# Performance work log

Measured on AMD Instinct MI355X. Metric: run time of the kernel, lower is better.

## Reference

```python
import jax, jax.numpy as jnp
import numpy as np

N = 100000      # nodes
E = 1600000     # edges
D_IN = 128      # input_dim
H = 256         # hidden_dim
L = 3           # num_layers
B = 64          # graphs per batch
BN_EPS = 1e-5


def setup_inputs() -> dict:
    key = jax.random.key(0)
    ks = jax.random.split(key, 8)
    x = jax.random.normal(ks[0], (N, D_IN), dtype=jnp.float32)
    edge_index = jax.random.randint(ks[1], (2, E), 0, N, dtype=jnp.int32)
    batch = jnp.sort(jax.random.randint(ks[2], (N,), 0, B, dtype=jnp.int32))
    W0 = jax.random.normal(ks[3], (D_IN, H), dtype=jnp.float32) / np.sqrt(D_IN)
    W_rest = jax.random.normal(ks[4], (L - 1, H, H), dtype=jnp.float32) / np.sqrt(H)
    b = jax.random.normal(ks[5], (L, H), dtype=jnp.float32) * 0.01
    gamma = 1.0 + jax.random.normal(ks[6], (L, H), dtype=jnp.float32) * 0.01
    beta = jax.random.normal(ks[7], (L, H), dtype=jnp.float32) * 0.01
    return {"x": x, "W0": W0, "W_rest": W_rest, "b": b, "gamma": gamma,
            "beta": beta, "edge_index": edge_index, "batch": batch}


def reference(x, W0, W_rest, b, gamma, beta, edge_index, batch):
    src, dst = edge_index[0], edge_index[1]
    # GCN symmetric normalization with self-loops: deg = in-degree + 1
    deg = jax.ops.segment_sum(jnp.ones((E,), x.dtype), dst, num_segments=N) + 1.0
    dis = jax.lax.rsqrt(deg)                   # deg^{-1/2}, [N]
    enorm = dis[src] * dis[dst]                # per-edge norm, [E]
    self_norm = (dis * dis)[:, None]           # self-loop norm = 1/deg, [N,1]

    def gcn_bn_relu(h, W, bb, g, be):
        h = h @ W                                                  # [N,H]
        agg = jax.ops.segment_sum(h[src] * enorm[:, None], dst, num_segments=N)
        h = agg + h * self_norm + bb                               # self-loop + bias
        # BatchNorm1d (training mode: batch stats, biased variance)
        m = h.mean(axis=0)
        v = h.var(axis=0)
        h = (h - m) * jax.lax.rsqrt(v + BN_EPS) * g + be
        return jax.nn.relu(h)                                      # dropout = identity (eval)

    h = gcn_bn_relu(x, W0, b[0], gamma[0], beta[0])
    for i in range(L - 1):
        h = gcn_bn_relu(h, W_rest[i], b[i + 1], gamma[i + 1], beta[i + 1])

    # segment pooling per graph (att_pool in the original is dead code: not returned)
    counts = jax.ops.segment_sum(jnp.ones((N,), h.dtype), batch, num_segments=B)
    mean_pool = jax.ops.segment_sum(h, batch, num_segments=B) / counts[:, None]
    max_pool = jax.ops.segment_max(h, batch, num_segments=B)
    return jnp.concatenate([mean_pool, max_pool], axis=1)          # [B, 2H]
```

## Files before the change

### kernel.cpp

```cpp
#include <hip/hip_runtime.h>
#include <hip/hip_bf16.h>
#include <stdint.h>


#define NN 100000
#define EE 1600000
#define BB 64
#define MPAD 100096
#define NBM (MPAD / 256)

typedef __attribute__((ext_vector_type(8))) short short8;
typedef __attribute__((ext_vector_type(4))) float f32x4;

__device__ __forceinline__ float bflo(uint32_t v){ return __uint_as_float(v << 16); }
__device__ __forceinline__ float bfhi(uint32_t v){ return __uint_as_float(v & 0xffff0000u); }
__device__ __forceinline__ uint32_t bfrne(float x){
  uint32_t u = __float_as_uint(x);
  return (u + 0x7fffu + ((u >> 16) & 1u)) >> 16;
}
__device__ __forceinline__ uint32_t bfpack(float a, float b){ return bfrne(a) | (bfrne(b) << 16); }
__device__ __forceinline__ float phi(long long p){
  return __uint_as_float((uint32_t)((unsigned long long)p >> 32));
}

__device__ __forceinline__ void gload_lds16(const void* g, void* l){
  __builtin_amdgcn_global_load_lds(
      (const __attribute__((address_space(1))) uint32_t*)g,
      (__attribute__((address_space(3))) uint32_t*)l, 16, 0, 0);
}

__global__ void k_deg(const int* __restrict__ dst, int* __restrict__ degi){
  for (int e = blockIdx.x * blockDim.x + threadIdx.x; e < EE; e += gridDim.x * blockDim.x)
    atomicAdd(&degi[dst[e]], 1);
}

__global__ void k_scan1(const int* __restrict__ degi, int* __restrict__ rp, int* __restrict__ bsum,
                        float* __restrict__ dis){
  __shared__ int lds[256];
  int b = blockIdx.x, t = threadIdx.x;
  int base = b * 1024 + t * 4;
  int v0 = (base + 0 < NN) ? degi[base + 0] : 0;
  int v1 = (base + 1 < NN) ? degi[base + 1] : 0;
  int v2 = (base + 2 < NN) ? degi[base + 2] : 0;
  int v3 = (base + 3 < NN) ? degi[base + 3] : 0;
  if (base + 0 < NN) dis[base + 0] = rsqrtf((float)v0 + 1.0f);
  if (base + 1 < NN) dis[base + 1] = rsqrtf((float)v1 + 1.0f);
  if (base + 2 < NN) dis[base + 2] = rsqrtf((float)v2 + 1.0f);
  if (base + 3 < NN) dis[base + 3] = rsqrtf((float)v3 + 1.0f);
  int s = v0 + v1 + v2 + v3;
  lds[t] = s; __syncthreads();
  for (int off = 1; off < 256; off <<= 1){
    int x = (t >= off) ? lds[t - off] : 0; __syncthreads();
    lds[t] += x; __syncthreads();
  }
  int excl = lds[t] - s;
  if (t == 255) bsum[b] = lds[255];
  if (base + 0 < NN) rp[base + 0] = excl;
  if (base + 1 < NN) rp[base + 1] = excl + v0;
  if (base + 2 < NN) rp[base + 2] = excl + v0 + v1;
  if (base + 3 < NN) rp[base + 3] = excl + v0 + v1 + v2;
}

__global__ void k_scan2(int* __restrict__ bsum, int nb){
  if (blockIdx.x == 0 && threadIdx.x == 0){
    int run = 0;
    for (int i = 0; i < nb; ++i){ int t = bsum[i]; bsum[i] = run; run += t; }
  }
}

__global__ void k_scan3(int* __restrict__ rp, int* __restrict__ cursor, const int* __restrict__ bsum){
  int b = blockIdx.x, t = threadIdx.x;
  int add = bsum[b];
  int base = b * 1024 + t * 4;
  #pragma unroll
  for (int j = 0; j < 4; ++j){
    int i = base + j;
    if (i < NN){ int v = rp[i] + add; rp[i] = v; cursor[i] = v; }
  }
  if (b == 0 && t == 0) rp[NN] = EE;
}

__global__ void k_fill(const int* __restrict__ src, const int* __restrict__ dst,
                       const float* __restrict__ dis, int* __restrict__ cursor,
                       long long* __restrict__ cp){
  for (int e = blockIdx.x * blockDim.x + threadIdx.x; e < EE; e += gridDim.x * blockDim.x){
    int s = src[e], d = dst[e];
    int pos = atomicAdd(&cursor[d], 1);
    float nrm = dis[s] * dis[d];
    long long v = (long long)(unsigned int)s | ((long long)(unsigned int)__float_as_uint(nrm) << 32);
    cp[pos] = v;
  }
}

__global__ void k_sort(const int* __restrict__ rp, long long* __restrict__ cp){
  int wid = (blockIdx.x * blockDim.x + threadIdx.x) >> 6;
  int lane = threadIdx.x & 63;
  if (wid >= NN) return;
  int beg = rp[wid], end = rp[wid + 1];
  int d = end - beg;
  if (d <= 1) return;
  if (d <= 64){
    long long key = (lane < d) ? cp[beg + lane] : 0x7fffffffffffffffLL;
    #pragma unroll
    for (int k = 2; k <= 64; k <<= 1){
      #pragma unroll
      for (int j = k >> 1; j > 0; j >>= 1){
        long long other = __shfl_xor(key, j);
        bool up = ((lane & k) == 0);
        bool keepMin = (((lane & j) == 0) == up);
        bool take = keepMin ? (other < key) : (other > key);
        if (take) key = other;
      }
    }
    if (lane < d) cp[beg + lane] = key;
  } else if (lane == 0){
    for (int i = beg + 1; i < end; ++i){
      long long k2 = cp[i];
      int j = i - 1;
      while (j >= beg && cp[j] > k2){ cp[j + 1] = cp[j]; --j; }
      cp[j + 1] = k2;
    }
  }
}

__global__ void k_prep(const float* __restrict__ W0, const float* __restrict__ Wr,
                       uint16_t* __restrict__ Wt0, uint16_t* __restrict__ Wt1,
                       uint16_t* __restrict__ Wt2,
                       const float* __restrict__ x, uint32_t* __restrict__ Xb){
  int b = blockIdx.x;
  if (b < 640){
    int i = b * 256 + threadIdx.x;
    if (i < 32768){
      int c = i >> 7, k = i & 127;
      Wt0[i] = (uint16_t)bfrne(W0[k * 256 + c]);
    } else if (i < 32768 + 131072){
      int j = i - 32768;
      int m = j >> 16, jj = j & 65535;
      int c = jj >> 8, k = jj & 255;
      uint16_t v = (uint16_t)bfrne(Wr[m * 65536 + k * 256 + c]);
      if (m == 0) Wt1[jj] = v; else Wt2[jj] = v;
    }
  } else {
    int i = (b - 640) * 256 + threadIdx.x;
    if (i >= MPAD * 64) return;
    int row = i >> 6;
    uint32_t r = 0u;
    if (row < NN){
      int col = (i & 63) * 2;
      r = bfpack(x[row * 128 + col], x[row * 128 + col + 1]);
    }
    Xb[i] = r;
  }
}

__global__ void k_agg256(const uint2* __restrict__ Xin, const int* __restrict__ rp,
                         const long long* __restrict__ cp, const float* __restrict__ dis,
                         uint2* __restrict__ Xout){
  int lane = threadIdx.x & 63;
  int slot = threadIdx.x >> 6;
  int row0 = blockIdx.x * 16 + slot;
  for (int rr = 0; rr < 4; ++rr){
    int row = row0 + rr * 4;
    if (row >= NN){
      if (row < MPAD)
        __builtin_nontemporal_store(0ull, (unsigned long long*)&Xout[(size_t)row * 64 + lane]);
      continue;
    }
    int beg = rp[row], end = rp[row + 1];
    float a0 = 0.f, a1 = 0.f, a2 = 0.f, a3 = 0.f;
    int e = beg;
    for (; e + 8 <= end; e += 8){
      long long p[8]; uint2 v[8];
      #pragma unroll
      for (int u = 0; u < 8; ++u) p[u] = __builtin_nontemporal_load(&cp[e + u]);
      #pragma unroll
      for (int u = 0; u < 8; ++u) v[u] = Xin[(size_t)(int)p[u] * 64 + lane];
      #pragma unroll
      for (int u = 0; u < 8; ++u){
        float w = phi(p[u]);
        a0 += w * bflo(v[u].x); a1 += w * bfhi(v[u].x);
        a2 += w * bflo(v[u].y); a3 += w * bfhi(v[u].y);
      }
    }
    for (; e < end; ++e){
      long long p0 = __builtin_nontemporal_load(&cp[e]);
      float w = phi(p0);
      uint2 v = Xin[(size_t)(int)p0 * 64 + lane];
      a0 += w * bflo(v.x); a1 += w * bfhi(v.x);
      a2 += w * bflo(v.y); a3 += w * bfhi(v.y);
    }
    float dv = dis[row]; float sn = dv * dv;
    uint2 vs = Xin[(size_t)row * 64 + lane];
    a0 += sn * bflo(vs.x); a1 += sn * bfhi(vs.x);
    a2 += sn * bflo(vs.y); a3 += sn * bfhi(vs.y);
    unsigned long long o = (unsigned long long)bfpack(a0, a1)
                         | ((unsigned long long)bfpack(a2, a3) << 32);
    __builtin_nontemporal_store(o, (unsigned long long*)&Xout[(size_t)row * 64 + lane]);
  }
}

__global__ void k_agg128(const uint2* __restrict__ Xin, const int* __restrict__ rp,
                         const long long* __restrict__ cp, const float* __restrict__ dis,
                         uint2* __restrict__ Xout){
  int lane = threadIdx.x & 63;
  int half = lane >> 5, j = lane & 31;
  int slot = threadIdx.x >> 6;
  int row0 = blockIdx.x * 16 + slot;
  for (int rr = 0; rr < 4; ++rr){
    int row = row0 + rr * 4;
    if (row >= NN){
      if (row < MPAD && half == 0)
        __builtin_nontemporal_store(0ull, (unsigned long long*)&Xout[(size_t)row * 32 + j]);
      continue;
    }
    int beg = rp[row], end = rp[row + 1];
    float a0 = 0.f, a1 = 0.f, a2 = 0.f, a3 = 0.f;
    int e = beg;
    for (; e + 8 <= end; e += 8){
      long long p[4]; uint2 v[4];
      #pragma unroll
      for (int u = 0; u < 4; ++u) p[u] = __builtin_nontemporal_load(&cp[e + u * 2 + half]);
      #pragma unroll
      for (int u = 0; u < 4; ++u) v[u] = Xin[(size_t)(int)p[u] * 32 + j];
      #pragma unroll
      for (int u = 0; u < 4; ++u){
        float w = phi(p[u]);
        a0 += w * bflo(v[u].x); a1 += w * bfhi(v[u].x);
        a2 += w * bflo(v[u].y); a3 += w * bfhi(v[u].y);
      }
    }
    for (; e < end; e += 2){
      int idx = e + half;
      bool ok = idx < end;
      long long p0 = cp[ok ? idx : end - 1];
      float w = ok ? phi(p0) : 0.f;
      uint2 v = Xin[(size_t)(int)p0 * 32 + j];
      a0 += w * bflo(v.x); a1 += w * bfhi(v.x);
      a2 += w * bflo(v.y); a3 += w * bfhi(v.y);
    }
    a0 += __shfl_xor(a0, 32); a1 += __shfl_xor(a1, 32);
    a2 += __shfl_xor(a2, 32); a3 += __shfl_xor(a3, 32);
    if (half == 0){
      float dv = dis[row]; float sn = dv * dv;
      uint2 vs = Xin[(size_t)row * 32 + j];
      a0 += sn * bflo(vs.x); a1 += sn * bfhi(vs.x);
      a2 += sn * bflo(vs.y); a3 += sn * bfhi(vs.y);
      unsigned long long o = (unsigned long long)bfpack(a0, a1)
                           | ((unsigned long long)bfpack(a2, a3) << 32);
      __builtin_nontemporal_store(o, (unsigned long long*)&Xout[(size_t)row * 32 + j]);
    }
  }
}

template<int K>
__global__ __launch_bounds__(512) void k_gemm(const uint16_t* __restrict__ A,
                                              const uint16_t* __restrict__ Bt,
                                              uint32_t* __restrict__ Cb,
                                              float* __restrict__ pstat){
  __shared__ __align__(16) uint16_t lA[2][8192];
  __shared__ __align__(16) uint16_t lB[2][4096];
  __shared__ float lp[8][128];
  int tid = threadIdx.x;
  int l = tid & 63;
  int bm = blockIdx.x, bn = blockIdx.y;

  f32x4 acc[4][4];
  #pragma unroll
  for (int m = 0; m < 4; ++m)
    #pragma unroll
    for (int n = 0; n < 4; ++n){ f32x4 z = {0.f,0.f,0.f,0.f}; acc[m][n] = z; }

  int w = tid >> 6, wr = w >> 1, wc = w & 1;
  int rbase = wr * 64, cbase = wc * 64;
  int lrow = l & 15, lk8 = l >> 4;

  auto stage = [&](int kt, int buf){
    #pragma unroll
    for (int i = 0; i < 2; ++i){
      int c = i * 512 + tid;
      int k8 = c >> 8, r = c & 255;
      size_t ga = (size_t)(bm * 256 + r) * K + kt * 32 + k8 * 8;
      gload_lds16((const char*)(A + ga), (char*)&lA[buf][c * 8]);
    }
    int k8b = tid >> 7, rb = tid & 127;
    size_t gb = (size_t)(bn * 128 + rb) * K + kt * 32 + k8b * 8;
    gload_lds16((const char*)(Bt + gb), (char*)&lB[buf][tid * 8]);
  };

  stage(0, 0);
  __syncthreads();
  constexpr int NT = K / 32;
  for (int kt = 0; kt < NT; ++kt){
    int cur = kt & 1;
    if (kt + 1 < NT) stage(kt + 1, cur ^ 1);
    short8 afr[4], bfr[4];
    #pragma unroll
    for (int m = 0; m < 4; ++m)
      afr[m] = *(const short8*)&lA[cur][(lk8 * 256 + rbase + m * 16 + lrow) * 8];
    #pragma unroll
    for (int n = 0; n < 4; ++n)
      bfr[n] = *(const short8*)&lB[cur][(lk8 * 128 + cbase + n * 16 + lrow) * 8];
    #pragma unroll
    for (int m = 0; m < 4; ++m)
      #pragma unroll
      for (int n = 0; n < 4; ++n)
        acc[m][n] = __builtin_amdgcn_mfma_f32_16x16x32_bf16(afr[m], bfr[n], acc[m][n], 0, 0, 0);
    __syncthreads();
  }

  int grow0 = bm * 256 + rbase + (l >> 4) * 4;
  int gcol0 = bn * 128 + cbase + (l & 15);
  uint16_t* C16 = (uint16_t*)Cb;
  float sa[4] = {0.f,0.f,0.f,0.f}, sb[4] = {0.f,0.f,0.f,0.f};
  #pragma unroll
  for (int m = 0; m < 4; ++m){
    #pragma unroll
    for (int n = 0; n < 4; ++n){
      int col = gcol0 + n * 16;
      int r0 = grow0 + m * 16;
      f32x4 v = acc[m][n];
      #pragma unroll
      for (int q = 0; q < 4; ++q){
        C16[(size_t)(r0 + q) * 256 + col] = (uint16_t)bfrne(v[q]);
        sa[n] += v[q]; sb[n] += v[q] * v[q];
      }
    }
  }
  #pragma unroll
  for (int n = 0; n < 4; ++n){
    sa[n] += __shfl_xor(sa[n], 16); sa[n] += __shfl_xor(sa[n], 32);
    sb[n] += __shfl_xor(sb[n], 16); sb[n] += __shfl_xor(sb[n], 32);
  }
  if (l < 16){
    #pragma unroll
    for (int n = 0; n < 4; ++n){
      lp[w][n * 16 + l] = sa[n];
      lp[w][64 + n * 16 + l] = sb[n];
    }
  }
  __syncthreads();
  if (tid < 256){
    int kind = tid >> 7, c = tid & 127;
    int wc2 = c >> 6, cc = c & 63;
    float v = lp[wc2][kind * 64 + cc] + lp[2 + wc2][kind * 64 + cc]
            + lp[4 + wc2][kind * 64 + cc] + lp[6 + wc2][kind * 64 + cc];
    pstat[(size_t)(bm * 2 + bn) * 256 + kind * 128 + c] = v;
  }
}

__global__ void k_finalize(const float* __restrict__ pstat, const float* __restrict__ gamma,
                           const float* __restrict__ beta, float* __restrict__ ss){
  int c = threadIdx.x;
  int bn = c >> 7, lc = c & 127;
  double s[8], s2[8];
  #pragma unroll
  for (int j = 0; j < 8; ++j){ s[j] = 0.; s2[j] = 0.; }
  int bm = 0;
  for (; bm + 8 <= NBM; bm += 8){
    #pragma unroll
    for (int j = 0; j < 8; ++j){
      const float* p = pstat + (size_t)((bm + j) * 2 + bn) * 256;
      s[j]  += (double)p[lc];
      s2[j] += (double)p[128 + lc];
    }
  }
  for (; bm < NBM; ++bm){
    const float* p = pstat + (size_t)(bm * 2 + bn) * 256;
    s[0]  += (double)p[lc];
    s2[0] += (double)p[128 + lc];
  }
  double S  = ((s[0]+s[1])+(s[2]+s[3]))  + ((s[4]+s[5])+(s[6]+s[7]));
  double S2 = ((s2[0]+s2[1])+(s2[2]+s2[3])) + ((s2[4]+s2[5])+(s2[6]+s2[7]));
  double mean = S / (double)NN;
  double var  = S2 / (double)NN - mean * mean;
  float rstd = rsqrtf((float)var + 1e-5f);
  float sc = gamma[c] * rstd;
  ss[c] = sc;
  ss[256 + c] = beta[c] - (float)mean * sc;
}

__global__ void k_bnapply(const uint4* __restrict__ Y, const float* __restrict__ ss,
                          uint4* __restrict__ X){
  int i = blockIdx.x * 256 + threadIdx.x;
  if (i >= MPAD * 32) return;
  uint4 v = Y[i];
  int c0 = (i & 31) * 8;
  float r0 = fmaxf(bflo(v.x) * ss[c0 + 0] + ss[256 + c0 + 0], 0.f);
  float r1 = fmaxf(bfhi(v.x) * ss[c0 + 1] + ss[256 + c0 + 1], 0.f);
  float r2 = fmaxf(bflo(v.y) * ss[c0 + 2] + ss[256 + c0 + 2], 0.f);
  float r3 = fmaxf(bfhi(v.y) * ss[c0 + 3] + ss[256 + c0 + 3], 0.f);
  float r4 = fmaxf(bflo(v.z) * ss[c0 + 4] + ss[256 + c0 + 4], 0.f);
  float r5 = fmaxf(bfhi(v.z) * ss[c0 + 5] + ss[256 + c0 + 5], 0.f);
  float r6 = fmaxf(bflo(v.w) * ss[c0 + 6] + ss[256 + c0 + 6], 0.f);
  float r7 = fmaxf(bfhi(v.w) * ss[c0 + 7] + ss[256 + c0 + 7], 0.f);
  uint4 o;
  o.x = bfpack(r0, r1); o.y = bfpack(r2, r3);
  o.z = bfpack(r4, r5); o.w = bfpack(r6, r7);
  X[i] = o;
}

__device__ __forceinline__ int segfind(const int* __restrict__ batch, int g){
  if (g <= 0) return 0;
  if (g >= BB) return NN;
  int lo = 0, hi = NN;
  while (lo < hi){ int mid = (lo + hi) >> 1; if (batch[mid] < g) lo = mid + 1; else hi = mid; }
  return lo;
}

__global__ void k_poolpart(const uint32_t* __restrict__ Y, const float* __restrict__ ss,
                           const int* __restrict__ batch, float* __restrict__ pb){
  int g = blockIdx.x, c = blockIdx.y, t = threadIdx.x;
  float sc0 = ss[2*t], sc1 = ss[2*t+1];
  float sh0 = ss[256+2*t], sh1 = ss[256+2*t+1];
  int s = segfind(batch, g), e = segfind(batch, g + 1);
  int len = e - s;
  int c0 = s + (int)(((long long)len * c) >> 3);
  int c1 = s + (int)(((long long)len * (c + 1)) >> 3);
  float sm0 = 0.f, sm1 = 0.f, mx0 = -1e30f, mx1 = -1e30f;
  #pragma unroll 4
  for (int r = c0; r < c1; ++r){
    uint32_t v = Y[(size_t)r * 128 + t];
    float a  = fmaxf(bflo(v) * sc0 + sh0, 0.f);
    float b2 = fmaxf(bfhi(v) * sc1 + sh1, 0.f);
    sm0 += a; sm1 += b2;
    mx0 = fmaxf(mx0, a); mx1 = fmaxf(mx1, b2);
  }
  float* p = pb + (size_t)(g * 8 + c) * 512;
  p[2 * t] = sm0; p[2 * t + 1] = sm1;
  p[256 + 2 * t] = mx0; p[256 + 2 * t + 1] = mx1;
}

__global__ void k_poolred(const float* __restrict__ pb, const int* __restrict__ batch,
                          float* __restrict__ out){
  int g = blockIdx.x, cc = threadIdx.x;
  float s = 0.f, m = -1e30f;
  #pragma unroll
  for (int c = 0; c < 8; ++c){
    const float* p = pb + (size_t)(g * 8 + c) * 512;
    s += p[cc];
    m = fmaxf(m, p[256 + cc]);
  }
  float inv = 1.0f / (float)(segfind(batch, g + 1) - segfind(batch, g));
  out[g * 512 + cc] = s * inv;
  out[g * 512 + 256 + cc] = m;
}

extern "C" void kernel_launch(void* const* d_in, const int* in_sizes, int n_in,
                              void* d_out, int out_size, void* d_ws, size_t ws_size,
                              hipStream_t stream){
  const float* x     = (const float*)d_in[0];
  const float* W0    = (const float*)d_in[1];
  const float* Wr    = (const float*)d_in[2];
  const float* gamma = (const float*)d_in[4];
  const float* beta  = (const float*)d_in[5];
  const int*   ei    = (const int*)d_in[6];
  const int*   batch = (const int*)d_in[7];
  const int* esrc = ei;
  const int* edst = ei + EE;
  float* out = (float*)d_out;

  char* base = (char*)d_ws;
  size_t off = 0;
  auto alloc = [&](size_t b)->char*{
    char* p = base + off; off = (off + b + 255) & ~(size_t)255; return p;
  };
  uint32_t* Xbuf = (uint32_t*)alloc((size_t)MPAD * 256 * 2);
  uint32_t* Xagg = (uint32_t*)alloc((size_t)MPAD * 256 * 2);
  uint32_t* Y    = (uint32_t*)alloc((size_t)MPAD * 256 * 2);
  uint16_t* Wt0  = (uint16_t*)alloc(256 * 128 * 2);
  uint16_t* Wt1  = (uint16_t*)alloc(256 * 256 * 2);
  uint16_t* Wt2  = (uint16_t*)alloc(256 * 256 * 2);
  int*   degi   = (int*)  alloc((size_t)NN * 4);
  float* dis    = (float*)alloc((size_t)NN * 4);
  int*   rp     = (int*)  alloc((size_t)(NN + 1) * 4);
  int*   cursor = (int*)  alloc((size_t)NN * 4);
  int*   bsum   = (int*)  alloc(128 * 4);
  long long* cp = (long long*)alloc((size_t)EE * 8);
  float* pstat  = (float*)alloc((size_t)NBM * 2 * 256 * 4);
  float* ss     = (float*)alloc(512 * 4);
  float* pb     = (float*)alloc((size_t)BB * 8 * 512 * 4);

  hipMemsetAsync(degi, 0, (size_t)NN * 4, stream);
  k_deg<<<2048, 256, 0, stream>>>(edst, degi);
  k_scan1<<<98, 256, 0, stream>>>(degi, rp, bsum, dis);
  k_scan2<<<1, 1, 0, stream>>>(bsum, 98);
  k_scan3<<<98, 256, 0, stream>>>(rp, cursor, bsum);
  k_fill<<<2048, 256, 0, stream>>>(esrc, edst, dis, cursor, cp);
  k_sort<<<NN / 4, 256, 0, stream>>>(rp, cp);
  k_prep<<<640 + MPAD * 64 / 256, 256, 0, stream>>>(W0, Wr, Wt0, Wt1, Wt2, x, Xbuf);

  k_agg128<<<MPAD / 16, 256, 0, stream>>>((const uint2*)Xbuf, rp, cp, dis, (uint2*)Xagg);
  k_gemm<128><<<dim3(NBM, 2), 512, 0, stream>>>((const uint16_t*)Xagg, Wt0, Y, pstat);
  k_finalize<<<1, 256, 0, stream>>>(pstat, gamma + 0, beta + 0, ss);
  k_bnapply<<<MPAD * 32 / 256, 256, 0, stream>>>((const uint4*)Y, ss, (uint4*)Xbuf);

  k_agg256<<<MPAD / 16, 256, 0, stream>>>((const uint2*)Xbuf, rp, cp, dis, (uint2*)Xagg);
  k_gemm<256><<<dim3(NBM, 2), 512, 0, stream>>>((const uint16_t*)Xagg, Wt1, Y, pstat);
  k_finalize<<<1, 256, 0, stream>>>(pstat, gamma + 256, beta + 256, ss);
  k_bnapply<<<MPAD * 32 / 256, 256, 0, stream>>>((const uint4*)Y, ss, (uint4*)Xbuf);

  k_agg256<<<MPAD / 16, 256, 0, stream>>>((const uint2*)Xbuf, rp, cp, dis, (uint2*)Xagg);
  k_gemm<256><<<dim3(NBM, 2), 512, 0, stream>>>((const uint16_t*)Xagg, Wt2, Y, pstat);
  k_finalize<<<1, 256, 0, stream>>>(pstat, gamma + 512, beta + 512, ss);

  k_poolpart<<<dim3(BB, 8), 128, 0, stream>>>(Y, ss, batch, pb);
  k_poolred<<<BB, 256, 0, stream>>>(pb, batch, out);
}
```

Baseline: 849.9 us.

## Fuse BatchNorm+ReLU into aggregation gather and drop separate bnapply and scan2 kernels

Removes the standalone k_bnapply pass by applying the per-channel scale/shift and ReLU (with bf16 rounding to match) on each gathered neighbor value inside k_agg256. It also folds the single-thread k_scan2 block-prefix into k_scan3 through a per-block LDS reduction, and switches cp loads from nontemporal to normal loads. This saves one full read/write pass of the 100k x 256 activation per layer and two launches. The cost is redundant BN math on every gathered edge (about 16x per node) plus an extra activation buffer.

```diff
diff --git a/kernel.cpp b/kernel.cpp
--- a/kernel.cpp
+++ b/kernel.cpp
@@ -21,6 +21,10 @@
 __device__ __forceinline__ uint32_t bfpack(float a, float b){ return bfrne(a) | (bfrne(b) << 16); }
 __device__ __forceinline__ float phi(long long p){
   return __uint_as_float((uint32_t)((unsigned long long)p >> 32));
+}
+__device__ __forceinline__ float bnr(float y, float sc, float sh){
+  float t = fmaxf(y * sc + sh, 0.f);
+  return __uint_as_float(bfrne(t) << 16);
 }
 
 __device__ __forceinline__ void gload_lds16(const void* g, void* l){
@@ -61,16 +65,16 @@
   if (base + 3 < NN) rp[base + 3] = excl + v0 + v1 + v2;
 }
 
-__global__ void k_scan2(int* __restrict__ bsum, int nb){
-  if (blockIdx.x == 0 && threadIdx.x == 0){
-    int run = 0;
-    for (int i = 0; i < nb; ++i){ int t = bsum[i]; bsum[i] = run; run += t; }
-  }
-}
-
 __global__ void k_scan3(int* __restrict__ rp, int* __restrict__ cursor, const int* __restrict__ bsum){
+  __shared__ int red[256];
   int b = blockIdx.x, t = threadIdx.x;
-  int add = bsum[b];
+  red[t] = (t < b && t < 98) ? bsum[t] : 0;
+  __syncthreads();
+  for (int off = 128; off > 0; off >>= 1){
+    if (t < off) red[t] += red[t + off];
+    __syncthreads();
+  }
+  int add = red[0];
   int base = b * 1024 + t * 4;
   #pragma unroll
   for (int j = 0; j < 4; ++j){
@@ -153,11 +157,13 @@
   }
 }
 
-__global__ void k_agg256(const uint2* __restrict__ Xin, const int* __restrict__ rp,
+__global__ void k_agg256(const uint2* __restrict__ Yin, const int* __restrict__ rp,
                          const long long* __restrict__ cp, const float* __restrict__ dis,
-                         uint2* __restrict__ Xout){
+                         const float* __restrict__ ss, uint2* __restrict__ Xout){
   int lane = threadIdx.x & 63;
   int slot = threadIdx.x >> 6;
+  float sc0 = ss[lane*4+0], sc1 = ss[lane*4+1], sc2 = ss[lane*4+2], sc3 = ss[lane*4+3];
+  float sh0 = ss[256+lane*4+0], sh1 = ss[256+lane*4+1], sh2 = ss[256+lane*4+2], sh3 = ss[256+lane*4+3];
   int row0 = blockIdx.x * 16 + slot;
   for (int rr = 0; rr < 4; ++rr){
     int row = row0 + rr * 4;
@@ -172,27 +178,33 @@
     for (; e + 8 <= end; e += 8){
       long long p[8]; uint2 v[8];
       #pragma unroll
-      for (int u = 0; u < 8; ++u) p[u] = __builtin_nontemporal_load(&cp[e + u]);
-      #pragma unroll
-      for (int u = 0; u < 8; ++u) v[u] = Xin[(size_t)(int)p[u] * 64 + lane];
+      for (int u = 0; u < 8; ++u) p[u] = cp[e + u];
+      #pragma unroll
+      for (int u = 0; u < 8; ++u) v[u] = Yin[(size_t)(int)p[u] * 64 + lane];
       #pragma unroll
       for (int u = 0; u < 8; ++u){
         float w = phi(p[u]);
-        a0 += w * bflo(v[u].x); a1 += w * bfhi(v[u].x);
-        a2 += w * bflo(v[u].y); a3 += w * bfhi(v[u].y);
+        a0 += w * bnr(bflo(v[u].x), sc0, sh0);
+        a1 += w * bnr(bfhi(v[u].x), sc1, sh1);
+        a2 += w * bnr(bflo(v[u].y), sc2, sh2);
+        a3 += w * bnr(bfhi(v[u].y), sc3, sh3);
       }
     }
     for (; e < end; ++e){
-      long long p0 = __builtin_nontemporal_load(&cp[e]);
+      long long p0 = cp[e];
       float w = phi(p0);
-      uint2 v = Xin[(size_t)(int)p0 * 64 + lane];
-      a0 += w * bflo(v.x); a1 += w * bfhi(v.x);
-      a2 += w * bflo(v.y); a3 += w * bfhi(v.y);
+      uint2 v = Yin[(size_t)(int)p0 * 64 + lane];
+      a0 += w * bnr(bflo(v.x), sc0, sh0);
+      a1 += w * bnr(bfhi(v.x), sc1, sh1);
+      a2 += w * bnr(bflo(v.y), sc2, sh2);
+      a3 += w * bnr(bfhi(v.y), sc3, sh3);
     }
     float dv = dis[row]; float sn = dv * dv;
-    uint2 vs = Xin[(size_t)row * 64 + lane];
-    a0 += sn * bflo(vs.x); a1 += sn * bfhi(vs.x);
-    a2 += sn * bflo(vs.y); a3 += sn * bfhi(vs.y);
+    uint2 vs = Yin[(size_t)row * 64 + lane];
+    a0 += sn * bnr(bflo(vs.x), sc0, sh0);
+    a1 += sn * bnr(bfhi(vs.x), sc1, sh1);
+    a2 += sn * bnr(bflo(vs.y), sc2, sh2);
+    a3 += sn * bnr(bfhi(vs.y), sc3, sh3);
     unsigned long long o = (unsigned long long)bfpack(a0, a1)
                          | ((unsigned long long)bfpack(a2, a3) << 32);
     __builtin_nontemporal_store(o, (unsigned long long*)&Xout[(size_t)row * 64 + lane]);
@@ -219,7 +231,7 @@
     for (; e + 8 <= end; e += 8){
       long long p[4]; uint2 v[4];
       #pragma unroll
-      for (int u = 0; u < 4; ++u) p[u] = __builtin_nontemporal_load(&cp[e + u * 2 + half]);
+      for (int u = 0; u < 4; ++u) p[u] = cp[e + u * 2 + half];
       #pragma unroll
       for (int u = 0; u < 4; ++u) v[u] = Xin[(size_t)(int)p[u] * 32 + j];
       #pragma unroll
@@ -377,26 +389,6 @@
   float sc = gamma[c] * rstd;
   ss[c] = sc;
   ss[256 + c] = beta[c] - (float)mean * sc;
-}
-
-__global__ void k_bnapply(const uint4* __restrict__ Y, const float* __restrict__ ss,
-                          uint4* __restrict__ X){
-  int i = blockIdx.x * 256 + threadIdx.x;
-  if (i >= MPAD * 32) return;
-  uint4 v = Y[i];
-  int c0 = (i & 31) * 8;
-  float r0 = fmaxf(bflo(v.x) * ss[c0 + 0] + ss[256 + c0 + 0], 0.f);
-  float r1 = fmaxf(bfhi(v.x) * ss[c0 + 1] + ss[256 + c0 + 1], 0.f);
-  float r2 = fmaxf(bflo(v.y) * ss[c0 + 2] + ss[256 + c0 + 2], 0.f);
-  float r3 = fmaxf(bfhi(v.y) * ss[c0 + 3] + ss[256 + c0 + 3], 0.f);
-  float r4 = fmaxf(bflo(v.z) * ss[c0 + 4] + ss[256 + c0 + 4], 0.f);
-  float r5 = fmaxf(bfhi(v.z) * ss[c0 + 5] + ss[256 + c0 + 5], 0.f);
-  float r6 = fmaxf(bflo(v.w) * ss[c0 + 6] + ss[256 + c0 + 6], 0.f);
-  float r7 = fmaxf(bfhi(v.w) * ss[c0 + 7] + ss[256 + c0 + 7], 0.f);
-  uint4 o;
-  o.x = bfpack(r0, r1); o.y = bfpack(r2, r3);
-  o.z = bfpack(r4, r5); o.w = bfpack(r6, r7);
-  X[i] = o;
 }
 
 __device__ __forceinline__ int segfind(const int* __restrict__ batch, int g){
@@ -464,9 +456,10 @@
   auto alloc = [&](size_t b)->char*{
     char* p = base + off; off = (off + b + 255) & ~(size_t)255; return p;
   };
-  uint32_t* Xbuf = (uint32_t*)alloc((size_t)MPAD * 256 * 2);
+  uint32_t* Xbuf = (uint32_t*)alloc((size_t)MPAD * 128 * 2);
   uint32_t* Xagg = (uint32_t*)alloc((size_t)MPAD * 256 * 2);
-  uint32_t* Y    = (uint32_t*)alloc((size_t)MPAD * 256 * 2);
+  uint32_t* Y1   = (uint32_t*)alloc((size_t)MPAD * 256 * 2);
+  uint32_t* Y2   = (uint32_t*)alloc((size_t)MPAD * 256 * 2);
   uint16_t* Wt0  = (uint16_t*)alloc(256 * 128 * 2);
   uint16_t* Wt1  = (uint16_t*)alloc(256 * 256 * 2);
   uint16_t* Wt2  = (uint16_t*)alloc(256 * 256 * 2);
@@ -483,26 +476,23 @@
   hipMemsetAsync(degi, 0, (size_t)NN * 4, stream);
   k_deg<<<2048, 256, 0, stream>>>(edst, degi);
   k_scan1<<<98, 256, 0, stream>>>(degi, rp, bsum, dis);
-  k_scan2<<<1, 1, 0, stream>>>(bsum, 98);
   k_scan3<<<98, 256, 0, stream>>>(rp, cursor, bsum);
   k_fill<<<2048, 256, 0, stream>>>(esrc, edst, dis, cursor, cp);
   k_sort<<<NN / 4, 256, 0, stream>>>(rp, cp);
   k_prep<<<640 + MPAD * 64 / 256, 256, 0, stream>>>(W0, Wr, Wt0, Wt1, Wt2, x, Xbuf);
 
   k_agg128<<<MPAD / 16, 256, 0, stream>>>((const uint2*)Xbuf, rp, cp, dis, (uint2*)Xagg);
-  k_gemm<128><<<dim3(NBM, 2), 512, 0, stream>>>((const uint16_t*)Xagg, Wt0, Y, pstat);
+  k_gemm<128><<<dim3(NBM, 2), 512, 0, stream>>>((const uint16_t*)Xagg, Wt0, Y1, pstat);
   k_finalize<<<1, 256, 0, stream>>>(pstat, gamma + 0, beta + 0, ss);
-  k_bnapply<<<MPAD * 32 / 256, 256, 0, stream>>>((const uint4*)Y, ss, (uint4*)Xbuf);
-
-  k_agg256<<<MPAD / 16, 256, 0, stream>>>((const uint2*)Xbuf, rp, cp, dis, (uint2*)Xagg);
-  k_gemm<256><<<dim3(NBM, 2), 512, 0, stream>>>((const uint16_t*)Xagg, Wt1, Y, pstat);
+
+  k_agg256<<<MPAD / 16, 256, 0, stream>>>((const uint2*)Y1, rp, cp, dis, ss, (uint2*)Xagg);
+  k_gemm<256><<<dim3(NBM, 2), 512, 0, stream>>>((const uint16_t*)Xagg, Wt1, Y2, pstat);
   k_finalize<<<1, 256, 0, stream>>>(pstat, gamma + 256, beta + 256, ss);
-  k_bnapply<<<MPAD * 32 / 256, 256, 0, stream>>>((const uint4*)Y, ss, (uint4*)Xbuf);
-
-  k_agg256<<<MPAD / 16, 256, 0, stream>>>((const uint2*)Xbuf, rp, cp, dis, (uint2*)Xagg);
-  k_gemm<256><<<dim3(NBM, 2), 512, 0, stream>>>((const uint16_t*)Xagg, Wt2, Y, pstat);
+
+  k_agg256<<<MPAD / 16, 256, 0, stream>>>((const uint2*)Y2, rp, cp, dis, ss, (uint2*)Xagg);
+  k_gemm<256><<<dim3(NBM, 2), 512, 0, stream>>>((const uint16_t*)Xagg, Wt2, Y1, pstat);
   k_finalize<<<1, 256, 0, stream>>>(pstat, gamma + 512, beta + 512, ss);
 
-  k_poolpart<<<dim3(BB, 8), 128, 0, stream>>>(Y, ss, batch, pb);
+  k_poolpart<<<dim3(BB, 8), 128, 0, stream>>>(Y1, ss, batch, pb);
   k_poolred<<<BB, 256, 0, stream>>>(pb, batch, out);
 }
```

Measured after the change: 772.5 us. 1.1x faster.
